# Kernel tuning notes

Hardware: AMD Instinct MI355X
Metric: run time of the kernel (lower is better)

Reference implementation:

```python
import jax, jax.numpy as jnp
import numpy as np

N = 100000        # nodes
E = 3200000       # edges (avg degree 32)
D_IN, D_H, D_OUT = 128, 128, 64
EPS = 1e-5        # BatchNorm eps


def setup_inputs() -> dict:
    key = jax.random.key(0)
    ks = jax.random.split(key, 12)
    s = 0.1
    return {
        "x": jax.random.normal(ks[0], (N, D_IN), jnp.float32),
        "edge_index": jax.random.randint(ks[1], (2, E), 0, N, jnp.int32),
        "W1": jax.random.normal(ks[2], (D_IN, D_H), jnp.float32) * s,
        "b1": jnp.zeros((D_H,), jnp.float32),
        "W2": jax.random.normal(ks[3], (D_H, D_H), jnp.float32) * s,
        "b2": jnp.zeros((D_H,), jnp.float32),
        "W3": jax.random.normal(ks[4], (D_H, D_OUT), jnp.float32) * s,
        "b3": jnp.zeros((D_OUT,), jnp.float32),
        "g1": jnp.ones((D_H,), jnp.float32),
        "be1": jnp.zeros((D_H,), jnp.float32),
        "g2": jnp.ones((D_H,), jnp.float32),
        "be2": jnp.zeros((D_H,), jnp.float32),
    }


def reference(x, edge_index, W1, b1, W2, b2, W3, b3, g1, be1, g2, be2):
    # GCNConv normalization: add self-loops, symmetric deg^-1/2 A deg^-1/2
    loop = jnp.arange(N, dtype=edge_index.dtype)
    src = jnp.concatenate([edge_index[0], loop])   # [E+N]
    dst = jnp.concatenate([edge_index[1], loop])   # [E+N]
    deg = jax.ops.segment_sum(jnp.ones(src.shape, x.dtype), dst, num_segments=N)
    dinv = jnp.where(deg > 0, jax.lax.rsqrt(deg), 0.0)
    norm = (dinv[src] * dinv[dst])[:, None]        # [E+N, 1]

    def conv(h, W, b):
        h = h @ W                                   # dense transform [N, d]
        msg = h[src] * norm                         # gather + scale [E+N, d]
        return jax.ops.segment_sum(msg, dst, num_segments=N) + b

    def bn(h, g, be):  # BatchNorm1d over nodes (batch stats, eval-style dropout)
        m = h.mean(axis=0)
        v = h.var(axis=0)
        return (h - m) * jax.lax.rsqrt(v + EPS) * g + be

    h = jax.nn.relu(bn(conv(x, W1, b1), g1, be1))
    h = jax.nn.relu(bn(conv(h, W2, b2), g2, be2))
    h = conv(h, W3, b3)
    return jax.nn.softmax(h, axis=1)
```

## Files before the change

kernel.cpp:

```cpp
#include <hip/hip_runtime.h>
#include <hip/hip_fp16.h>

constexpr int   NN   = 100000;
constexpr int   NE   = 3200000;
constexpr float BN_EPS = 1e-5f;

constexpr int MG_B  = (NN / 32 + 3) / 4;
constexpr int NB    = (NN + 127) / 128;
constexpr int HB    = 256;
constexpr int CHUNK = NE / HB;

typedef _Float16 half8 __attribute__((ext_vector_type(8)));
typedef float    floatx16 __attribute__((ext_vector_type(16)));

__global__ __launch_bounds__(256) void k_wprep_all(const float* __restrict__ W1,
                                                   const float* __restrict__ W2,
                                                   const float* __restrict__ W3,
                                                   _Float16* __restrict__ Wt1,
                                                   _Float16* __restrict__ Wt2,
                                                   _Float16* __restrict__ Wt3) {
  int idx = blockIdx.x * 256 + threadIdx.x;
  if (idx < 16384) {
    int k = idx >> 7, n = idx & 127;
    Wt1[n * 128 + k] = (_Float16)W1[idx];
  } else if (idx < 32768) {
    int j = idx - 16384, k = j >> 7, n = j & 127;
    Wt2[n * 128 + k] = (_Float16)W2[j];
  } else if (idx < 40960) {
    int j = idx - 32768, k = j >> 6, n = j & 63;
    Wt3[n * 128 + k] = (_Float16)W3[j];
  }
}

__global__ __launch_bounds__(256) void k_f1(const int* __restrict__ dst,
                                            int* __restrict__ blkhist,
                                            const float* __restrict__ x,
                                            const _Float16* __restrict__ Wt1,
                                            _Float16* __restrict__ C) {
  __shared__ int h[NB];
  if (blockIdx.x < MG_B) {
    int wid  = (blockIdx.x * 256 + threadIdx.x) >> 6;
    int lane = threadIdx.x & 63;
    if (wid >= NN / 32) return;
    const int m = lane & 31;
    const int q = lane >> 5;
    const int row0 = wid * 32;
    const float* Arow = x + (size_t)(row0 + m) * 128 + q * 8;

    floatx16 acc[4] = {};
#pragma unroll
    for (int s = 0; s < 8; ++s) {
      float4 a0 = *(const float4*)(Arow + 16 * s);
      float4 a1 = *(const float4*)(Arow + 16 * s + 4);
      half8 af;
      af[0] = (_Float16)a0.x; af[1] = (_Float16)a0.y;
      af[2] = (_Float16)a0.z; af[3] = (_Float16)a0.w;
      af[4] = (_Float16)a1.x; af[5] = (_Float16)a1.y;
      af[6] = (_Float16)a1.z; af[7] = (_Float16)a1.w;
#pragma unroll
      for (int ct = 0; ct < 4; ++ct) {
        half8 bf = *(const half8*)(Wt1 + (size_t)(ct * 32 + m) * 128 + q * 8 + 16 * s);
        acc[ct] = __builtin_amdgcn_mfma_f32_32x32x16_f16(af, bf, acc[ct], 0, 0, 0);
      }
    }
#pragma unroll
    for (int ct = 0; ct < 4; ++ct)
#pragma unroll
      for (int r = 0; r < 16; ++r) {
        int row = (r & 3) + 8 * (r >> 2) + 4 * q;
        C[(size_t)(row0 + row) * 128 + ct * 32 + m] = (_Float16)acc[ct][r];
      }
  } else {
    int j = blockIdx.x - MG_B;
    int t = threadIdx.x;
    for (int b = t; b < NB; b += 256) h[b] = 0;
    __syncthreads();
    int base = j * CHUNK;
    for (int e = base + t; e < base + CHUNK; e += 256)
      atomicAdd(&h[dst[e] >> 7], 1);
    __syncthreads();
    for (int b = t; b < NB; b += 256) blkhist[j * NB + b] = h[b];
  }
}

__global__ __launch_bounds__(256) void k_scan_bkt_a(const int* __restrict__ blkhist,
                                                    int* __restrict__ blkbase,
                                                    int* __restrict__ total) {
  int wid  = (blockIdx.x * 256 + threadIdx.x) >> 6;
  int lane = threadIdx.x & 63;
  if (wid >= NB) return;
  int i0 = lane * 4;
  int v0 = blkhist[(i0 + 0) * NB + wid];
  int v1 = blkhist[(i0 + 1) * NB + wid];
  int v2 = blkhist[(i0 + 2) * NB + wid];
  int v3 = blkhist[(i0 + 3) * NB + wid];
  int lt = v0 + v1 + v2 + v3;
  int inc = lt;
#pragma unroll
  for (int off = 1; off < 64; off <<= 1) {
    int xx = __shfl_up(inc, off);
    if (lane >= off) inc += xx;
  }
  int exc = inc - lt;
  blkbase[(i0 + 0) * NB + wid] = exc;
  blkbase[(i0 + 1) * NB + wid] = exc + v0;
  blkbase[(i0 + 2) * NB + wid] = exc + v0 + v1;
  blkbase[(i0 + 3) * NB + wid] = exc + v0 + v1 + v2;
  if (lane == 63) total[wid] = inc;
}

__global__ __launch_bounds__(1024) void k_scan_bkt_b(const int* __restrict__ total,
                                                     int* __restrict__ bbase) {
  __shared__ int s[1024];
  int t = threadIdx.x;
  int v = (t < NB) ? total[t] : 0;
  s[t] = v;
  __syncthreads();
  for (int off = 1; off < 1024; off <<= 1) {
    int xx = (t >= off) ? s[t - off] : 0;
    __syncthreads();
    s[t] += xx;
    __syncthreads();
  }
  if (t < NB) bbase[t] = s[t] - v;
  if (t == NB - 1) bbase[NB] = s[t];
}

__global__ __launch_bounds__(256) void k_scatter(const int* __restrict__ ei,
                                                 const int* __restrict__ bbase,
                                                 const int* __restrict__ blkbase,
                                                 int* __restrict__ ebuf) {
  __shared__ int cur[NB];
  int i = blockIdx.x;
  int t = threadIdx.x;
  for (int b = t; b < NB; b += 256) cur[b] = bbase[b] + blkbase[i * NB + b];
  __syncthreads();
  int base = i * CHUNK;
  for (int e = base + t; e < base + CHUNK; e += 256) {
    int s = ei[e];
    int d = ei[NE + e];
    int b = d >> 7;
    int pos = atomicAdd(&cur[b], 1);
    ebuf[pos] = s | ((d & 127) << 17);
  }
}

__global__ __launch_bounds__(256) void k_bucket(const int* __restrict__ bbase,
                                                const int* __restrict__ ebuf,
                                                int* __restrict__ rowptr,
                                                float* __restrict__ dinv,
                                                int* __restrict__ csrc) {
  __shared__ int degL[128];
  __shared__ int sc[128];
  __shared__ int curL[128];
  int b = blockIdx.x;
  int t = threadIdx.x;
  int e0 = bbase[b], e1 = bbase[b + 1];
  if (t < 128) degL[t] = 0;
  __syncthreads();
  for (int e = e0 + t; e < e1; e += 256)
    atomicAdd(&degL[ebuf[e] >> 17], 1);
  __syncthreads();
  if (t < 128) sc[t] = degL[t];
  __syncthreads();
  for (int off = 1; off < 128; off <<= 1) {
    int xx = 0;
    if (t < 128 && t >= off) xx = sc[t - off];
    __syncthreads();
    if (t < 128) sc[t] += xx;
    __syncthreads();
  }
  if (t < 128) {
    int node = b * 128 + t;
    if (node < NN) {
      int d = degL[t];
      int exc = sc[t] - d;
      rowptr[node] = e0 + exc;
      dinv[node] = rsqrtf((float)(d + 1));
      curL[t] = exc;
    }
  }
  if (b == NB - 1 && t == 0) rowptr[NN] = NE;
  __syncthreads();
  for (int e = e0 + t; e < e1; e += 256) {
    int p = ebuf[e];
    int pos = atomicAdd(&curL[p >> 17], 1);
    csrc[e0 + pos] = p & 0x1FFFF;
  }
}

template <int BN_>
__global__ __launch_bounds__(256) void k_mgemm(const _Float16* __restrict__ A,
                                               const _Float16* __restrict__ Wt,
                                               const float* __restrict__ scale,
                                               const float* __restrict__ shift,
                                               const float* __restrict__ dinv,
                                               _Float16* __restrict__ C) {
  constexpr int NCT = BN_ / 32;
  int wid  = (blockIdx.x * 256 + threadIdx.x) >> 6;
  int lane = threadIdx.x & 63;
  if (wid >= NN / 32) return;
  const int m = lane & 31;
  const int q = lane >> 5;
  const int row0 = wid * 32;

  const _Float16* Arow = A + (size_t)(row0 + m) * 128 + q * 8;

  floatx16 acc[NCT] = {};

#pragma unroll
  for (int s = 0; s < 8; ++s) {
    half8 raw = *(const half8*)(Arow + 16 * s);
    int k0 = 16 * s + q * 8;
    half8 af;
#pragma unroll
    for (int j = 0; j < 8; ++j) {
      float a = fmaxf(fmaf((float)raw[j], scale[k0 + j], shift[k0 + j]), 0.f);
      af[j] = (_Float16)a;
    }
#pragma unroll
    for (int ct = 0; ct < NCT; ++ct) {
      half8 bf = *(const half8*)(Wt + (size_t)(ct * 32 + m) * 128 + q * 8 + 16 * s);
      acc[ct] = __builtin_amdgcn_mfma_f32_32x32x16_f16(af, bf, acc[ct], 0, 0, 0);
    }
  }

#pragma unroll
  for (int ct = 0; ct < NCT; ++ct)
#pragma unroll
    for (int r = 0; r < 16; ++r) {
      int row = (r & 3) + 8 * (r >> 2) + 4 * q;
      float dv = dinv[row0 + row];
      C[(size_t)(row0 + row) * BN_ + ct * 32 + m] = (_Float16)(acc[ct][r] * dv);
    }
}

template <bool SRCSCALE>
__global__ __launch_bounds__(256) void k_agg128(const __half* __restrict__ H,
                                                const float* __restrict__ dinv,
                                                const int* __restrict__ rowptr,
                                                const int* __restrict__ srcs,
                                                __half2* __restrict__ out) {
  int wid  = (blockIdx.x * 256 + threadIdx.x) >> 6;
  int lane = threadIdx.x & 63;
  if (wid >= NN) return;
  const __half2* Hp = (const __half2*)H;
  float di = dinv[wid];
  float2 self = __half22float2(Hp[(size_t)wid * 64 + lane]);
  float2 acc;
  if (SRCSCALE) { acc.x = self.x * di; acc.y = self.y * di; }
  else          { acc = self; }
  int beg = rowptr[wid], end = rowptr[wid + 1];
  int e = beg;
  int end8 = beg + ((end - beg) & ~7);
  for (; e < end8; e += 8) {
    int s0 = srcs[e+0], s1 = srcs[e+1], s2 = srcs[e+2], s3 = srcs[e+3];
    int s4 = srcs[e+4], s5 = srcs[e+5], s6 = srcs[e+6], s7 = srcs[e+7];
    __half2 v0 = Hp[(size_t)s0 * 64 + lane];
    __half2 v1 = Hp[(size_t)s1 * 64 + lane];
    __half2 v2 = Hp[(size_t)s2 * 64 + lane];
    __half2 v3 = Hp[(size_t)s3 * 64 + lane];
    __half2 v4 = Hp[(size_t)s4 * 64 + lane];
    __half2 v5 = Hp[(size_t)s5 * 64 + lane];
    __half2 v6 = Hp[(size_t)s6 * 64 + lane];
    __half2 v7 = Hp[(size_t)s7 * 64 + lane];
    float2 f0 = __half22float2(v0), f1 = __half22float2(v1);
    float2 f2 = __half22float2(v2), f3 = __half22float2(v3);
    float2 f4 = __half22float2(v4), f5 = __half22float2(v5);
    float2 f6 = __half22float2(v6), f7 = __half22float2(v7);
    if (SRCSCALE) {
      float d0 = dinv[s0], d1 = dinv[s1], d2 = dinv[s2], d3 = dinv[s3];
      float d4 = dinv[s4], d5 = dinv[s5], d6 = dinv[s6], d7 = dinv[s7];
      acc.x = fmaf(f0.x, d0, acc.x); acc.y = fmaf(f0.y, d0, acc.y);
      acc.x = fmaf(f1.x, d1, acc.x); acc.y = fmaf(f1.y, d1, acc.y);
      acc.x = fmaf(f2.x, d2, acc.x); acc.y = fmaf(f2.y, d2, acc.y);
      acc.x = fmaf(f3.x, d3, acc.x); acc.y = fmaf(f3.y, d3, acc.y);
      acc.x = fmaf(f4.x, d4, acc.x); acc.y = fmaf(f4.y, d4, acc.y);
      acc.x = fmaf(f5.x, d5, acc.x); acc.y = fmaf(f5.y, d5, acc.y);
      acc.x = fmaf(f6.x, d6, acc.x); acc.y = fmaf(f6.y, d6, acc.y);
      acc.x = fmaf(f7.x, d7, acc.x); acc.y = fmaf(f7.y, d7, acc.y);
    } else {
      acc.x += (f0.x + f1.x) + (f2.x + f3.x) + (f4.x + f5.x) + (f6.x + f7.x);
      acc.y += (f0.y + f1.y) + (f2.y + f3.y) + (f4.y + f5.y) + (f6.y + f7.y);
    }
  }
  for (; e < end; ++e) {
    int s = srcs[e];
    float2 f = __half22float2(Hp[(size_t)s * 64 + lane]);
    if (SRCSCALE) {
      float dd = dinv[s];
      acc.x = fmaf(f.x, dd, acc.x); acc.y = fmaf(f.y, dd, acc.y);
    } else {
      acc.x += f.x; acc.y += f.y;
    }
  }
  out[(size_t)wid * 64 + lane] = __floats2half2_rn(acc.x * di, acc.y * di);
}

__global__ __launch_bounds__(256) void k_agg64_softmax(const __half* __restrict__ H,
                                                       const float* __restrict__ dinv,
                                                       const int* __restrict__ rowptr,
                                                       const int* __restrict__ srcs,
                                                       const float* __restrict__ b3,
                                                       float* __restrict__ out) {
  int wid  = (blockIdx.x * 256 + threadIdx.x) >> 6;
  int lane = threadIdx.x & 63;
  if (wid >= NN) return;
  float acc = __half2float(H[(size_t)wid * 64 + lane]);
  int beg = rowptr[wid], end = rowptr[wid + 1];
  int e = beg;
  int end8 = beg + ((end - beg) & ~7);
  for (; e < end8; e += 8) {
    float v0 = __half2float(H[(size_t)srcs[e+0] * 64 + lane]);
    float v1 = __half2float(H[(size_t)srcs[e+1] * 64 + lane]);
    float v2 = __half2float(H[(size_t)srcs[e+2] * 64 + lane]);
    float v3 = __half2float(H[(size_t)srcs[e+3] * 64 + lane]);
    float v4 = __half2float(H[(size_t)srcs[e+4] * 64 + lane]);
    float v5 = __half2float(H[(size_t)srcs[e+5] * 64 + lane]);
    float v6 = __half2float(H[(size_t)srcs[e+6] * 64 + lane]);
    float v7 = __half2float(H[(size_t)srcs[e+7] * 64 + lane]);
    acc += (v0 + v1) + (v2 + v3) + (v4 + v5) + (v6 + v7);
  }
  for (; e < end; ++e)
    acc += __half2float(H[(size_t)srcs[e] * 64 + lane]);
  acc = acc * dinv[wid] + b3[lane];

  float m = acc;
#pragma unroll
  for (int off = 32; off > 0; off >>= 1) m = fmaxf(m, __shfl_xor(m, off));
  float ev = __expf(acc - m);
  float s = ev;
#pragma unroll
  for (int off = 32; off > 0; off >>= 1) s += __shfl_xor(s, off);
  out[(size_t)wid * 64 + lane] = ev / s;
}

__global__ __launch_bounds__(256) void k_stats(const __half2* __restrict__ H2,
                                               float* __restrict__ S1,
                                               float* __restrict__ S2) {
  int t = threadIdx.x;
  int p = t & 63;
  int r = t >> 6;
  float2 s1 = {0.f, 0.f}, s2 = {0.f, 0.f};
  for (int row = blockIdx.x * 4 + r; row < NN; row += gridDim.x * 4) {
    float2 v = __half22float2(H2[(size_t)row * 64 + p]);
    s1.x += v.x; s1.y += v.y;
    s2.x += v.x * v.x; s2.y += v.y * v.y;
  }
  __shared__ float2 l1[256], l2[256];
  l1[t] = s1; l2[t] = s2;
  __syncthreads();
  if (t < 128) {
    l1[t].x += l1[t+128].x; l1[t].y += l1[t+128].y;
    l2[t].x += l2[t+128].x; l2[t].y += l2[t+128].y;
  }
  __syncthreads();
  if (t < 64) {
    float2 a1 = l1[t], b1 = l1[t+64];
    float2 a2 = l2[t], b2 = l2[t+64];
    atomicAdd(&S1[2*p+0], a1.x + b1.x);
    atomicAdd(&S1[2*p+1], a1.y + b1.y);
    atomicAdd(&S2[2*p+0], a2.x + b2.x);
    atomicAdd(&S2[2*p+1], a2.y + b2.y);
  }
}

__global__ void k_finalize(const float* __restrict__ S1, const float* __restrict__ S2,
                           const float* __restrict__ g,  const float* __restrict__ be,
                           float* __restrict__ scale,    float* __restrict__ shift) {
  int t = threadIdx.x;
  float mean = S1[t] * (1.0f / NN);
  float var  = S2[t] * (1.0f / NN) - mean * mean;
  float is   = rsqrtf(var + BN_EPS);
  float sc   = g[t] * is;
  scale[t] = sc;
  shift[t] = be[t] - mean * sc;
}

extern "C" void kernel_launch(void* const* d_in, const int* in_sizes, int n_in,
                              void* d_out, int out_size, void* d_ws, size_t ws_size,
                              hipStream_t stream) {
  (void)in_sizes; (void)n_in; (void)out_size; (void)ws_size;
  const float* x   = (const float*)d_in[0];
  const int*   ei  = (const int*)d_in[1];
  const float* W1  = (const float*)d_in[2];
  const float* W2  = (const float*)d_in[4];
  const float* W3  = (const float*)d_in[6];
  const float* b3  = (const float*)d_in[7];
  const float* g1  = (const float*)d_in[8];
  const float* be1 = (const float*)d_in[9];
  const float* g2  = (const float*)d_in[10];
  const float* be2 = (const float*)d_in[11];
  float* out = (float*)d_out;

  char* ws = (char*)d_ws;
  size_t off = 0;
  auto take = [&](size_t bytes) -> char* {
    char* p = ws + off;
    off = (off + bytes + 255) & ~(size_t)255;
    return p;
  };
  float* S1a    = (float*)take(128 * 4);
  float* S2a    = (float*)take(128 * 4);
  float* S1b    = (float*)take(128 * 4);
  float* S2b    = (float*)take(128 * 4);
  size_t zero_bytes = off;
  float* scale1 = (float*)take(128 * 4);
  float* shift1 = (float*)take(128 * 4);
  float* scale2 = (float*)take(128 * 4);
  float* shift2 = (float*)take(128 * 4);
  float* dinv   = (float*)take((size_t)NN * 4);
  int*   rowptr = (int*)  take((size_t)(NN + 1) * 4);
  int*   bbase  = (int*)  take((size_t)(NB + 1) * 4);
  int*   total  = (int*)  take((size_t)NB * 4);
  int*   blkhist= (int*)  take((size_t)HB * NB * 4);
  int*   blkbase= (int*)  take((size_t)HB * NB * 4);
  int*   ebuf   = (int*)  take((size_t)NE * 4);
  int*   csrc   = (int*)  take((size_t)NE * 4);
  _Float16* Wt1 = (_Float16*)take((size_t)128 * 128 * 2);
  _Float16* Wt2 = (_Float16*)take((size_t)128 * 128 * 2);
  _Float16* Wt3 = (_Float16*)take((size_t)64 * 128 * 2);
  _Float16* Hf  = (_Float16*)take((size_t)NN * 128 * 2);
  _Float16* hB  = (_Float16*)take((size_t)NN * 128 * 2);

  (void)hipMemsetAsync(d_ws, 0, zero_bytes, stream);

  const int mgB  = MG_B;
  const int aggB = (NN + 3) / 4;
  const int scanAB = (NB + 3) / 4;

  k_wprep_all<<<160, 256, 0, stream>>>(W1, W2, W3, Wt1, Wt2, Wt3);

  k_f1<<<MG_B + HB, 256, 0, stream>>>(ei + NE, blkhist, x, Wt1, Hf);

  k_scan_bkt_a<<<scanAB, 256, 0, stream>>>(blkhist, blkbase, total);
  k_scan_bkt_b<<<1, 1024, 0, stream>>>(total, bbase);
  k_scatter<<<HB, 256, 0, stream>>>(ei, bbase, blkbase, ebuf);
  k_bucket<<<NB, 256, 0, stream>>>(bbase, ebuf, rowptr, dinv, csrc);

  k_agg128<true><<<aggB, 256, 0, stream>>>((const __half*)Hf, dinv, rowptr, csrc, (__half2*)hB);
  k_stats<<<1024, 256, 0, stream>>>((const __half2*)hB, S1a, S2a);
  k_finalize<<<1, 128, 0, stream>>>(S1a, S2a, g1, be1, scale1, shift1);

  k_mgemm<128><<<mgB, 256, 0, stream>>>(hB, Wt2, scale1, shift1, dinv, Hf);
  k_agg128<false><<<aggB, 256, 0, stream>>>((const __half*)Hf, dinv, rowptr, csrc, (__half2*)hB);
  k_stats<<<1024, 256, 0, stream>>>((const __half2*)hB, S1b, S2b);
  k_finalize<<<1, 128, 0, stream>>>(S1b, S2b, g2, be2, scale2, shift2);

  k_mgemm<64><<<mgB, 256, 0, stream>>>(hB, Wt3, scale2, shift2, dinv, Hf);
  k_agg64_softmax<<<aggB, 256, 0, stream>>>((const __half*)Hf, dinv, rowptr, csrc, b3, out);
}
```

Before: 732.4 us.

## Vectorize aggregation gathers with 16-byte loads across edge-parallel lane groups

The 128-wide and 64-wide aggregation kernels now split each wavefront into lane groups that each handle different edges. Each lane loads 8 halves with one 16-byte access instead of one half2 or half per lane, and the group partials are combined with cross-lane shuffles before the store. The softmax is redone in this layout, with each lane holding 8 values. Separately, the bucket kernel scatters sorted sources into shared memory and writes them back to global memory coalesced, falling back to direct global scatter when a bucket exceeds capacity. The aim is fewer, wider gather transactions and more edges in flight per wave, at the cost of extra shuffles and a large shared-memory buffer that may lower bucket-kernel occupancy.

After: 685.3 us. -6.4%, faster.

```diff
diff --git a/kernel.cpp b/kernel.cpp
--- a/kernel.cpp
+++ b/kernel.cpp
@@ -9,9 +9,11 @@
 constexpr int NB    = (NN + 127) / 128;
 constexpr int HB    = 256;
 constexpr int CHUNK = NE / HB;
+constexpr int BKT_CAP = 5120;
 
 typedef _Float16 half8 __attribute__((ext_vector_type(8)));
 typedef float    floatx16 __attribute__((ext_vector_type(16)));
+typedef float    floatx8  __attribute__((ext_vector_type(8)));
 
 __global__ __launch_bounds__(256) void k_wprep_all(const float* __restrict__ W1,
                                                    const float* __restrict__ W2,
@@ -153,9 +155,11 @@
   __shared__ int degL[128];
   __shared__ int sc[128];
   __shared__ int curL[128];
+  __shared__ int sorted[BKT_CAP];
   int b = blockIdx.x;
   int t = threadIdx.x;
   int e0 = bbase[b], e1 = bbase[b + 1];
+  int cnt = e1 - e0;
   if (t < 128) degL[t] = 0;
   __syncthreads();
   for (int e = e0 + t; e < e1; e += 256)
@@ -182,10 +186,20 @@
   }
   if (b == NB - 1 && t == 0) rowptr[NN] = NE;
   __syncthreads();
-  for (int e = e0 + t; e < e1; e += 256) {
-    int p = ebuf[e];
-    int pos = atomicAdd(&curL[p >> 17], 1);
-    csrc[e0 + pos] = p & 0x1FFFF;
+  if (cnt <= BKT_CAP) {
+    for (int e = e0 + t; e < e1; e += 256) {
+      int p = ebuf[e];
+      int pos = atomicAdd(&curL[p >> 17], 1);
+      sorted[pos] = p & 0x1FFFF;
+    }
+    __syncthreads();
+    for (int i = t; i < cnt; i += 256) csrc[e0 + i] = sorted[i];
+  } else {
+    for (int e = e0 + t; e < e1; e += 256) {
+      int p = ebuf[e];
+      int pos = atomicAdd(&curL[p >> 17], 1);
+      csrc[e0 + pos] = p & 0x1FFFF;
+    }
   }
 }
 
@@ -244,57 +258,56 @@
   int wid  = (blockIdx.x * 256 + threadIdx.x) >> 6;
   int lane = threadIdx.x & 63;
   if (wid >= NN) return;
-  const __half2* Hp = (const __half2*)H;
+  const int g  = lane >> 4;
+  const int sl = lane & 15;
+  const _Float16* Hb = (const _Float16*)H + (size_t)sl * 8;
   float di = dinv[wid];
-  float2 self = __half22float2(Hp[(size_t)wid * 64 + lane]);
-  float2 acc;
-  if (SRCSCALE) { acc.x = self.x * di; acc.y = self.y * di; }
-  else          { acc = self; }
+  floatx8 acc = {};
+  if (g == 0) {
+    half8 h = *(const half8*)(Hb + (size_t)wid * 128);
+    float ds = SRCSCALE ? di : 1.f;
+#pragma unroll
+    for (int j = 0; j < 8; ++j) acc[j] = (float)h[j] * ds;
+  }
   int beg = rowptr[wid], end = rowptr[wid + 1];
-  int e = beg;
-  int end8 = beg + ((end - beg) & ~7);
-  for (; e < end8; e += 8) {
-    int s0 = srcs[e+0], s1 = srcs[e+1], s2 = srcs[e+2], s3 = srcs[e+3];
-    int s4 = srcs[e+4], s5 = srcs[e+5], s6 = srcs[e+6], s7 = srcs[e+7];
-    __half2 v0 = Hp[(size_t)s0 * 64 + lane];
-    __half2 v1 = Hp[(size_t)s1 * 64 + lane];
-    __half2 v2 = Hp[(size_t)s2 * 64 + lane];
-    __half2 v3 = Hp[(size_t)s3 * 64 + lane];
-    __half2 v4 = Hp[(size_t)s4 * 64 + lane];
-    __half2 v5 = Hp[(size_t)s5 * 64 + lane];
-    __half2 v6 = Hp[(size_t)s6 * 64 + lane];
-    __half2 v7 = Hp[(size_t)s7 * 64 + lane];
-    float2 f0 = __half22float2(v0), f1 = __half22float2(v1);
-    float2 f2 = __half22float2(v2), f3 = __half22float2(v3);
-    float2 f4 = __half22float2(v4), f5 = __half22float2(v5);
-    float2 f6 = __half22float2(v6), f7 = __half22float2(v7);
+  int e = beg + g;
+  for (; e + 4 < end; e += 8) {
+    int s0 = srcs[e];
+    int s1 = srcs[e + 4];
+    half8 h0 = *(const half8*)(Hb + (size_t)s0 * 128);
+    half8 h1 = *(const half8*)(Hb + (size_t)s1 * 128);
     if (SRCSCALE) {
-      float d0 = dinv[s0], d1 = dinv[s1], d2 = dinv[s2], d3 = dinv[s3];
-      float d4 = dinv[s4], d5 = dinv[s5], d6 = dinv[s6], d7 = dinv[s7];
-      acc.x = fmaf(f0.x, d0, acc.x); acc.y = fmaf(f0.y, d0, acc.y);
-      acc.x = fmaf(f1.x, d1, acc.x); acc.y = fmaf(f1.y, d1, acc.y);
-      acc.x = fmaf(f2.x, d2, acc.x); acc.y = fmaf(f2.y, d2, acc.y);
-      acc.x = fmaf(f3.x, d3, acc.x); acc.y = fmaf(f3.y, d3, acc.y);
-      acc.x = fmaf(f4.x, d4, acc.x); acc.y = fmaf(f4.y, d4, acc.y);
-      acc.x = fmaf(f5.x, d5, acc.x); acc.y = fmaf(f5.y, d5, acc.y);
-      acc.x = fmaf(f6.x, d6, acc.x); acc.y = fmaf(f6.y, d6, acc.y);
-      acc.x = fmaf(f7.x, d7, acc.x); acc.y = fmaf(f7.y, d7, acc.y);
+      float d0 = dinv[s0], d1 = dinv[s1];
+#pragma unroll
+      for (int j = 0; j < 8; ++j) {
+        acc[j] = fmaf((float)h0[j], d0, acc[j]);
+        acc[j] = fmaf((float)h1[j], d1, acc[j]);
+      }
     } else {
-      acc.x += (f0.x + f1.x) + (f2.x + f3.x) + (f4.x + f5.x) + (f6.x + f7.x);
-      acc.y += (f0.y + f1.y) + (f2.y + f3.y) + (f4.y + f5.y) + (f6.y + f7.y);
-    }
-  }
-  for (; e < end; ++e) {
-    int s = srcs[e];
-    float2 f = __half22float2(Hp[(size_t)s * 64 + lane]);
-    if (SRCSCALE) {
-      float dd = dinv[s];
-      acc.x = fmaf(f.x, dd, acc.x); acc.y = fmaf(f.y, dd, acc.y);
-    } else {
-      acc.x += f.x; acc.y += f.y;
-    }
-  }
-  out[(size_t)wid * 64 + lane] = __floats2half2_rn(acc.x * di, acc.y * di);
+#pragma unroll
+      for (int j = 0; j < 8; ++j)
+        acc[j] += (float)h0[j] + (float)h1[j];
+    }
+  }
+  if (e < end) {
+    int s0 = srcs[e];
+    half8 h0 = *(const half8*)(Hb + (size_t)s0 * 128);
+    float d0 = SRCSCALE ? dinv[s0] : 1.f;
+#pragma unroll
+    for (int j = 0; j < 8; ++j) acc[j] = fmaf((float)h0[j], d0, acc[j]);
+  }
+#pragma unroll
+  for (int j = 0; j < 8; ++j) {
+    acc[j] += __shfl_xor(acc[j], 16);
+    acc[j] += __shfl_xor(acc[j], 32);
+  }
+  if (g == 0) {
+    __half2 o[4];
+#pragma unroll
+    for (int j = 0; j < 4; ++j)
+      o[j] = __floats2half2_rn(acc[2 * j] * di, acc[2 * j + 1] * di);
+    *(int4*)(out + (size_t)wid * 64 + sl * 4) = *(const int4*)o;
+  }
 }
 
 __global__ __launch_bounds__(256) void k_agg64_softmax(const __half* __restrict__ H,
@@ -306,33 +319,65 @@
   int wid  = (blockIdx.x * 256 + threadIdx.x) >> 6;
   int lane = threadIdx.x & 63;
   if (wid >= NN) return;
-  float acc = __half2float(H[(size_t)wid * 64 + lane]);
+  const int g  = lane >> 3;
+  const int sl = lane & 7;
+  const _Float16* Hb = (const _Float16*)H + (size_t)sl * 8;
+  floatx8 acc = {};
+  if (g == 0) {
+    half8 h = *(const half8*)(Hb + (size_t)wid * 64);
+#pragma unroll
+    for (int j = 0; j < 8; ++j) acc[j] = (float)h[j];
+  }
   int beg = rowptr[wid], end = rowptr[wid + 1];
-  int e = beg;
-  int end8 = beg + ((end - beg) & ~7);
-  for (; e < end8; e += 8) {
-    float v0 = __half2float(H[(size_t)srcs[e+0] * 64 + lane]);
-    float v1 = __half2float(H[(size_t)srcs[e+1] * 64 + lane]);
-    float v2 = __half2float(H[(size_t)srcs[e+2] * 64 + lane]);
-    float v3 = __half2float(H[(size_t)srcs[e+3] * 64 + lane]);
-    float v4 = __half2float(H[(size_t)srcs[e+4] * 64 + lane]);
-    float v5 = __half2float(H[(size_t)srcs[e+5] * 64 + lane]);
-    float v6 = __half2float(H[(size_t)srcs[e+6] * 64 + lane]);
-    float v7 = __half2float(H[(size_t)srcs[e+7] * 64 + lane]);
-    acc += (v0 + v1) + (v2 + v3) + (v4 + v5) + (v6 + v7);
-  }
-  for (; e < end; ++e)
-    acc += __half2float(H[(size_t)srcs[e] * 64 + lane]);
-  acc = acc * dinv[wid] + b3[lane];
-
-  float m = acc;
-#pragma unroll
-  for (int off = 32; off > 0; off >>= 1) m = fmaxf(m, __shfl_xor(m, off));
-  float ev = __expf(acc - m);
-  float s = ev;
-#pragma unroll
-  for (int off = 32; off > 0; off >>= 1) s += __shfl_xor(s, off);
-  out[(size_t)wid * 64 + lane] = ev / s;
+  int e = beg + g;
+  for (; e + 8 < end; e += 16) {
+    int s0 = srcs[e];
+    int s1 = srcs[e + 8];
+    half8 h0 = *(const half8*)(Hb + (size_t)s0 * 64);
+    half8 h1 = *(const half8*)(Hb + (size_t)s1 * 64);
+#pragma unroll
+    for (int j = 0; j < 8; ++j)
+      acc[j] += (float)h0[j] + (float)h1[j];
+  }
+  if (e < end) {
+    int s0 = srcs[e];
+    half8 h0 = *(const half8*)(Hb + (size_t)s0 * 64);
+#pragma unroll
+    for (int j = 0; j < 8; ++j) acc[j] += (float)h0[j];
+  }
+#pragma unroll
+  for (int j = 0; j < 8; ++j) {
+    acc[j] += __shfl_xor(acc[j], 8);
+    acc[j] += __shfl_xor(acc[j], 16);
+    acc[j] += __shfl_xor(acc[j], 32);
+  }
+  float di = dinv[wid];
+  float4 bA = *(const float4*)(b3 + sl * 8);
+  float4 bB = *(const float4*)(b3 + sl * 8 + 4);
+  float v[8];
+  v[0] = acc[0] * di + bA.x; v[1] = acc[1] * di + bA.y;
+  v[2] = acc[2] * di + bA.z; v[3] = acc[3] * di + bA.w;
+  v[4] = acc[4] * di + bB.x; v[5] = acc[5] * di + bB.y;
+  v[6] = acc[6] * di + bB.z; v[7] = acc[7] * di + bB.w;
+  float m = v[0];
+#pragma unroll
+  for (int j = 1; j < 8; ++j) m = fmaxf(m, v[j]);
+  m = fmaxf(m, __shfl_xor(m, 1));
+  m = fmaxf(m, __shfl_xor(m, 2));
+  m = fmaxf(m, __shfl_xor(m, 4));
+  float s = 0.f;
+#pragma unroll
+  for (int j = 0; j < 8; ++j) { v[j] = __expf(v[j] - m); s += v[j]; }
+  s += __shfl_xor(s, 1);
+  s += __shfl_xor(s, 2);
+  s += __shfl_xor(s, 4);
+  float inv = 1.0f / s;
+  if (g == 0) {
+    float4 oA = {v[0] * inv, v[1] * inv, v[2] * inv, v[3] * inv};
+    float4 oB = {v[4] * inv, v[5] * inv, v[6] * inv, v[7] * inv};
+    *(float4*)(out + (size_t)wid * 64 + sl * 8)     = oA;
+    *(float4*)(out + (size_t)wid * 64 + sl * 8 + 4) = oB;
+  }
 }
 
 __global__ __launch_bounds__(256) void k_stats(const __half2* __restrict__ H2,
```
